# Performance work log

Measured on AMD Instinct MI355X. Metric: run time of the kernel, lower is better.

Reference implementation:

```python
import jax, jax.numpy as jnp
import numpy as np

D = 9  # nodefeat_n1 = 3 (resnet feat) + 6 (pos)


def _lstm_scan(x, Wih, Whh, bih, bhh, reverse=False):
    # x: [T, B, D] -> hidden states [T, B, D]; torch gate order i,f,g,o
    B = x.shape[1]
    def step(carry, xt):
        h, c = carry
        g = xt @ Wih.T + bih + h @ Whh.T + bhh
        i = jax.nn.sigmoid(g[:, :D])
        f = jax.nn.sigmoid(g[:, D:2*D])
        gg = jnp.tanh(g[:, 2*D:3*D])
        o = jax.nn.sigmoid(g[:, 3*D:])
        c = f * c + i * gg
        h = o * jnp.tanh(c)
        return (h, c), h
    init = (jnp.zeros((B, D), x.dtype), jnp.zeros((B, D), x.dtype))
    _, hs = jax.lax.scan(step, init, x, reverse=reverse)
    return hs


def _forward(nodes_feature, pos, attmat, msg_W, msg_b, gru_Wih, gru_Whh, gru_bih, gru_bhh,
             ro1_W, ro1_b, ro2_W, ro2_b, lf_Wih, lf_Whh, lf_bih, lf_bhh,
             lb_Wih, lb_Whh, lb_bih, lb_bhh, lr1_W, lr1_b, lr2_W, lr2_b, num_rec):
    node_feat = jnp.concatenate([nodes_feature, pos], axis=-1)  # [N,T,M,D]
    N, T, M, _ = node_feat.shape
    # valid_node_num = num_rec[b, 0] in the original code
    valid = (jnp.arange(M)[None, :] < num_rec[:, 0:1]).astype(node_feat.dtype)  # [N,M]
    att = attmat * valid[:, None, None, :]  # zero out invalid source nodes q
    src = node_feat  # message sources (h_w)
    hv = node_feat   # GRU hidden (h_v)
    hidden = node_feat
    for _ in range(2):  # iterN = 2 message-passing rounds
        msg = src @ msg_W.T + msg_b                    # [N,T,M,D] message_fc
        m = jnp.einsum('btnq,btqd->btnd', att, msg)    # attention-weighted sum over q
        # single-step GRU cell (torch gate order r,z,n)
        gx = m @ gru_Wih.T + gru_bih
        gh = hv @ gru_Whh.T + gru_bhh
        r = jax.nn.sigmoid(gx[..., :D] + gh[..., :D])
        z = jax.nn.sigmoid(gx[..., D:2*D] + gh[..., D:2*D])
        n = jnp.tanh(gx[..., 2*D:] + r * gh[..., 2*D:])
        h_new = (1.0 - z) * n + z * hv
        hidden = h_new * valid[:, None, :, None]       # invalid nodes never updated -> stay zero
        src = hidden
        hv = hidden
    vmask = valid[:, None, :, None]
    # per-frame readout (pred_label0)
    p0 = jax.nn.relu(hidden @ ro1_W.T + ro1_b) @ ro2_W.T + ro2_b
    pred_label0 = p0 * vmask
    # bidirectional LSTM over time, batched over (batch, node)
    x = hidden.transpose(1, 0, 2, 3).reshape(T, N * M, D)  # [T, N*M, D]
    hf = _lstm_scan(x, lf_Wih, lf_Whh, lf_bih, lf_bhh, reverse=False)
    hb = _lstm_scan(x, lb_Wih, lb_Whh, lb_bih, lb_bhh, reverse=True)
    out = jnp.concatenate([hf, hb], axis=-1).reshape(T, N, M, 2 * D).transpose(1, 0, 2, 3)
    p = jax.nn.relu(out @ lr1_W.T + lr1_b) @ lr2_W.T + lr2_b
    pred_label = p * vmask
    return pred_label, pred_label0


def setup_inputs() -> dict:
    key = jax.random.key(0)
    ks = jax.random.split(key, 32)
    N, T, M = 8192, 20, 6
    def u(k, shape, fan_in):
        s = 1.0 / np.sqrt(fan_in).astype(np.float32)
        return jax.random.uniform(k, shape, jnp.float32, -s, s)
    return {
        "nodes_feature": jax.random.normal(ks[0], (N, T, M, 3), jnp.float32),
        "pos": jax.random.normal(ks[1], (N, T, M, 6), jnp.float32),
        "attmat": jax.random.uniform(ks[2], (N, T, M, M), jnp.float32),
        "msg_W": u(ks[3], (D, D), D), "msg_b": u(ks[4], (D,), D),
        "gru_Wih": u(ks[5], (3 * D, D), D), "gru_Whh": u(ks[6], (3 * D, D), D),
        "gru_bih": u(ks[7], (3 * D,), D), "gru_bhh": u(ks[8], (3 * D,), D),
        "ro1_W": u(ks[9], (D, D), D), "ro1_b": u(ks[10], (D,), D),
        "ro2_W": u(ks[11], (7, D), D), "ro2_b": u(ks[12], (7,), D),
        "lf_Wih": u(ks[13], (4 * D, D), D), "lf_Whh": u(ks[14], (4 * D, D), D),
        "lf_bih": u(ks[15], (4 * D,), D), "lf_bhh": u(ks[16], (4 * D,), D),
        "lb_Wih": u(ks[17], (4 * D, D), D), "lb_Whh": u(ks[18], (4 * D, D), D),
        "lb_bih": u(ks[19], (4 * D,), D), "lb_bhh": u(ks[20], (4 * D,), D),
        "lr1_W": u(ks[21], (D, 2 * D), 2 * D), "lr1_b": u(ks[22], (D,), 2 * D),
        "lr2_W": u(ks[23], (7, D), D), "lr2_b": u(ks[24], (7,), D),
        "num_rec": jax.random.randint(ks[25], (N, T), 1, M + 1),
    }


def reference(nodes_feature, pos, attmat, msg_W, msg_b, gru_Wih, gru_Whh, gru_bih, gru_bhh,
              ro1_W, ro1_b, ro2_W, ro2_b, lf_Wih, lf_Whh, lf_bih, lf_bhh,
              lb_Wih, lb_Whh, lb_bih, lb_bhh, lr1_W, lr1_b, lr2_W, lr2_b, num_rec):
    return _forward(nodes_feature, pos, attmat, msg_W, msg_b, gru_Wih, gru_Whh, gru_bih, gru_bhh,
                    ro1_W, ro1_b, ro2_W, ro2_b, lf_Wih, lf_Whh, lf_bih, lf_bhh,
                    lb_Wih, lb_Whh, lb_bih, lb_bhh, lr1_W, lr1_b, lr2_W, lr2_b, num_rec)
```

## Files before the change

### kernel.cpp

```cpp
#include <hip/hip_runtime.h>

#define N_    8192
#define T_    20
#define M_    6
#define D_    9
#define NM_   (N_*M_)
#define NT_   (N_*T_)
#define NTM7_ (N_*T_*M_*7)

#define LOG2E 1.44269504088896f

typedef __attribute__((ext_vector_type(2))) float v2f;

__device__ __forceinline__ float sigm(float x){
    return __builtin_amdgcn_rcpf(1.f + __builtin_amdgcn_exp2f(-LOG2E * x));
}
__device__ __forceinline__ float tanh_(float x){
    return fmaf(2.f, __builtin_amdgcn_rcpf(1.f + __builtin_amdgcn_exp2f(-2.f*LOG2E * x)), -1.f);
}
__device__ __forceinline__ v2f splat(float s){ return (v2f){s, s}; }
__device__ __forceinline__ v2f sigm2(v2f x){ v2f r; r.x = sigm(x.x); r.y = sigm(x.y); return r; }
__device__ __forceinline__ v2f tanh2(v2f x){ v2f r; r.x = tanh_(x.x); r.y = tanh_(x.y); return r; }
__device__ __forceinline__ v2f relu2(v2f x){ v2f r; r.x = fmaxf(x.x,0.f); r.y = fmaxf(x.y,0.f); return r; }

__global__ __launch_bounds__(64) void k_gnn(
    const float* __restrict__ nf,
    const float* __restrict__ pos,
    const float* __restrict__ am,
    const float* __restrict__ msgW, const float* __restrict__ msgb,
    const float* __restrict__ gWih, const float* __restrict__ gWhh,
    const float* __restrict__ gbih, const float* __restrict__ gbhh,
    const float* __restrict__ ro1W, const float* __restrict__ ro1b,
    const float* __restrict__ ro2W, const float* __restrict__ ro2b,
    const int*   __restrict__ numrec,
    float* __restrict__ hid,
    float* __restrict__ out0)
{
    __shared__ v2f mbuf[11 * 58];

    const int lane = threadIdx.x & 63;
    const int g    = lane / 6;
    const int i    = lane - g * 6;
    const int gB   = g * 58;
    const bool lactive = (lane < 60);

    const int wbase = blockIdx.x * 20;
    const int ntA = lactive ? (wbase + g)      : 0;
    const int ntB = lactive ? (wbase + 10 + g) : 0;
    const int nA = ntA / T_, tA = ntA - nA * T_;
    const int nB = ntB / T_, tB = ntB - nB * T_;

    v2f s[D_];
    {
        const float* pA = nf + (size_t)ntA * 18 + i * 3;
        const float* pB = nf + (size_t)ntB * 18 + i * 3;
        #pragma unroll
        for (int k = 0; k < 3; ++k) { s[k].x = pA[k]; s[k].y = pB[k]; }
    }
    {
        const float2* pA = (const float2*)(pos + (size_t)ntA * 36 + i * 6);
        const float2* pB = (const float2*)(pos + (size_t)ntB * 36 + i * 6);
        #pragma unroll
        for (int k = 0; k < 3; ++k) {
            float2 a = pA[k], b = pB[k];
            s[3 + 2*k]     = (v2f){a.x, b.x};
            s[3 + 2*k + 1] = (v2f){a.y, b.y};
        }
    }
    v2f attr[M_];
    {
        const float2* pA = (const float2*)(am + (size_t)ntA * 36 + i * 6);
        const float2* pB = (const float2*)(am + (size_t)ntB * 36 + i * 6);
        #pragma unroll
        for (int k = 0; k < 3; ++k) {
            float2 a = pA[k], b = pB[k];
            attr[2*k]     = (v2f){a.x, b.x};
            attr[2*k + 1] = (v2f){a.y, b.y};
        }
    }
    const int nrA = numrec[nA * T_];
    const int nrB = numrec[nB * T_];
    #pragma unroll
    for (int q = 0; q < M_; ++q) {
        attr[q].x *= (q < nrA) ? 1.f : 0.f;
        attr[q].y *= (q < nrB) ? 1.f : 0.f;
    }
    v2f vmi; vmi.x = (i < nrA) ? 1.f : 0.f; vmi.y = (i < nrB) ? 1.f : 0.f;

    #pragma unroll
    for (int it = 0; it < 2; ++it) {
        #pragma unroll
        for (int d = 0; d < D_; ++d) {
            v2f a = splat(msgb[d]);
            #pragma unroll
            for (int k = 0; k < D_; ++k) a += s[k] * msgW[d*9 + k];
            mbuf[gB + d*6 + i] = a;
        }
        v2f mm[D_];
        #pragma unroll
        for (int d = 0; d < D_; ++d) {
            const float4* rp = (const float4*)&mbuf[gB + d*6];
            float4 p0 = rp[0], p1 = rp[1], p2 = rp[2];
            v2f a = attr[0] * (v2f){p0.x, p0.y};
            a += attr[1] * (v2f){p0.z, p0.w};
            a += attr[2] * (v2f){p1.x, p1.y};
            a += attr[3] * (v2f){p1.z, p1.w};
            a += attr[4] * (v2f){p2.x, p2.y};
            a += attr[5] * (v2f){p2.z, p2.w};
            mm[d] = a;
        }
        v2f grz[18], gxn[9], ghn[9];
        #pragma unroll
        for (int j = 0; j < 18; ++j) {
            v2f a = splat(gbih[j] + gbhh[j]);
            #pragma unroll
            for (int k = 0; k < D_; ++k) {
                a += mm[k] * gWih[j*9 + k];
                a += s[k]  * gWhh[j*9 + k];
            }
            grz[j] = a;
        }
        #pragma unroll
        for (int j = 0; j < 9; ++j) {
            v2f ax = splat(gbih[18 + j]), ah = splat(gbhh[18 + j]);
            #pragma unroll
            for (int k = 0; k < D_; ++k) {
                ax += mm[k] * gWih[(18 + j)*9 + k];
                ah += s[k]  * gWhh[(18 + j)*9 + k];
            }
            gxn[j] = ax; ghn[j] = ah;
        }
        #pragma unroll
        for (int d = 0; d < D_; ++d) {
            v2f r  = sigm2(grz[d]);
            v2f z  = sigm2(grz[9 + d]);
            v2f nn = tanh2(gxn[d] + r * ghn[d]);
            s[d] = vmi * ((splat(1.f) - z) * nn + z * s[d]);
        }
    }

    if (lactive) {
        float* hpA = hid + (size_t)(nA * M_ + i) * (T_ * D_) + tA * D_;
        float* hpB = hid + (size_t)(nB * M_ + i) * (T_ * D_) + tB * D_;
        #pragma unroll
        for (int d = 0; d < D_; ++d) { hpA[d] = s[d].x; hpB[d] = s[d].y; }
    }

    v2f q9[D_];
    #pragma unroll
    for (int d = 0; d < D_; ++d) {
        v2f a = splat(ro1b[d]);
        #pragma unroll
        for (int k = 0; k < D_; ++k) a += s[k] * ro1W[d*9 + k];
        q9[d] = relu2(a);
    }
    if (lactive) {
        float* opA = out0 + (size_t)ntA * 42 + i * 7;
        float* opB = out0 + (size_t)ntB * 42 + i * 7;
        #pragma unroll
        for (int j = 0; j < 7; ++j) {
            v2f a = splat(ro2b[j]);
            #pragma unroll
            for (int k = 0; k < D_; ++k) a += q9[k] * ro2W[j*9 + k];
            a *= vmi;
            opA[j] = a.x; opB[j] = a.y;
        }
    }
}

#define CPB 14

__global__ __launch_bounds__(128) void k_lstm(
    const float* __restrict__ hid,
    const float* __restrict__ fWih, const float* __restrict__ fWhh,
    const float* __restrict__ fbih, const float* __restrict__ fbhh,
    const float* __restrict__ bWih, const float* __restrict__ bWhh,
    const float* __restrict__ bbih, const float* __restrict__ bbhh,
    const float* __restrict__ lr1W, const float* __restrict__ lr1b,
    const float* __restrict__ lr2W, const float* __restrict__ lr2b,
    const int*   __restrict__ numrec,
    float* __restrict__ out)
{
    __shared__ float hst[16 * 404];
    __shared__ float hxs[16 * 20];

    const int lane = threadIdx.x & 63;
    const int wib  = threadIdx.x >> 6;
    const int grp0 = lane / 9;
    const int d    = lane - grp0 * 9;
    const int row  = wib * 8 + grp0;
    const int grp  = (grp0 < 7) ? grp0 : 6;

    bool active = (lane < 63);
    int ci = blockIdx.x * CPB + wib * 7 + grp;
    active = active && (ci < NM_);
    const int nm = active ? ci : 0;

    const float* xb = hid + (size_t)nm * (T_ * D_);
    const int crow = row * 20;
    const int hrow = row * 404;

    {
        float wxi[9], wxf[9], wxg[9], wxo[9], whi[9], whf[9], whg[9], who[9];
        #pragma unroll
        for (int k = 0; k < 9; ++k) {
            wxi[k] = fWih[(d     )*9 + k];  whi[k] = fWhh[(d     )*9 + k];
            wxf[k] = fWih[(9  + d)*9 + k];  whf[k] = fWhh[(9  + d)*9 + k];
            wxg[k] = fWih[(18 + d)*9 + k];  whg[k] = fWhh[(18 + d)*9 + k];
            wxo[k] = fWih[(27 + d)*9 + k];  who[k] = fWhh[(27 + d)*9 + k];
        }
        const float bi = fbih[d]      + fbhh[d];
        const float bf = fbih[9 + d]  + fbhh[9 + d];
        const float bg = fbih[18 + d] + fbhh[18 + d];
        const float bo = fbih[27 + d] + fbhh[27 + d];

        hxs[crow + 2*d] = 0.f;
        float h = 0.f, c = 0.f;
        for (int t = 0; t < T_; ++t) {
            hxs[crow + 2*d + 1] = xb[t*9 + d];
            float gi = bi, gf = bf, gg = bg, go = bo;
            #pragma unroll
            for (int j = 0; j < 8; j += 2) {
                float4 v = *(const float4*)&hxs[crow + 2*j];
                gi = fmaf(v.x, whi[j], fmaf(v.y, wxi[j], gi));
                gf = fmaf(v.x, whf[j], fmaf(v.y, wxf[j], gf));
                gg = fmaf(v.x, whg[j], fmaf(v.y, wxg[j], gg));
                go = fmaf(v.x, who[j], fmaf(v.y, wxo[j], go));
                gi = fmaf(v.z, whi[j+1], fmaf(v.w, wxi[j+1], gi));
                gf = fmaf(v.z, whf[j+1], fmaf(v.w, wxf[j+1], gf));
                gg = fmaf(v.z, whg[j+1], fmaf(v.w, wxg[j+1], gg));
                go = fmaf(v.z, who[j+1], fmaf(v.w, wxo[j+1], go));
            }
            {
                float2 v = *(const float2*)&hxs[crow + 16];
                gi = fmaf(v.x, whi[8], fmaf(v.y, wxi[8], gi));
                gf = fmaf(v.x, whf[8], fmaf(v.y, wxf[8], gf));
                gg = fmaf(v.x, whg[8], fmaf(v.y, wxg[8], gg));
                go = fmaf(v.x, who[8], fmaf(v.y, wxo[8], go));
            }
            c = sigm(gf) * c + sigm(gi) * tanh_(gg);
            h = sigm(go) * tanh_(c);
            hst[hrow + t*20 + d] = h;
            hxs[crow + 2*d] = h;
        }
    }

    {
        float wxi[9], wxf[9], wxg[9], wxo[9], whi[9], whf[9], whg[9], who[9];
        #pragma unroll
        for (int k = 0; k < 9; ++k) {
            wxi[k] = bWih[(d     )*9 + k];  whi[k] = bWhh[(d     )*9 + k];
            wxf[k] = bWih[(9  + d)*9 + k];  whf[k] = bWhh[(9  + d)*9 + k];
            wxg[k] = bWih[(18 + d)*9 + k];  whg[k] = bWhh[(18 + d)*9 + k];
            wxo[k] = bWih[(27 + d)*9 + k];  who[k] = bWhh[(27 + d)*9 + k];
        }
        const float bi = bbih[d]      + bbhh[d];
        const float bf = bbih[9 + d]  + bbhh[9 + d];
        const float bg = bbih[18 + d] + bbhh[18 + d];
        const float bo = bbih[27 + d] + bbhh[27 + d];

        hxs[crow + 2*d] = 0.f;
        float h = 0.f, c = 0.f;
        for (int tt = T_ - 1; tt >= 0; --tt) {
            hxs[crow + 2*d + 1] = xb[tt*9 + d];
            float gi = bi, gf = bf, gg = bg, go = bo;
            #pragma unroll
            for (int j = 0; j < 8; j += 2) {
                float4 v = *(const float4*)&hxs[crow + 2*j];
                gi = fmaf(v.x, whi[j], fmaf(v.y, wxi[j], gi));
                gf = fmaf(v.x, whf[j], fmaf(v.y, wxf[j], gf));
                gg = fmaf(v.x, whg[j], fmaf(v.y, wxg[j], gg));
                go = fmaf(v.x, who[j], fmaf(v.y, wxo[j], go));
                gi = fmaf(v.z, whi[j+1], fmaf(v.w, wxi[j+1], gi));
                gf = fmaf(v.z, whf[j+1], fmaf(v.w, wxf[j+1], gf));
                gg = fmaf(v.z, whg[j+1], fmaf(v.w, wxg[j+1], gg));
                go = fmaf(v.z, who[j+1], fmaf(v.w, wxo[j+1], go));
            }
            {
                float2 v = *(const float2*)&hxs[crow + 16];
                gi = fmaf(v.x, whi[8], fmaf(v.y, wxi[8], gi));
                gf = fmaf(v.x, whf[8], fmaf(v.y, wxf[8], gf));
                gg = fmaf(v.x, whg[8], fmaf(v.y, wxg[8], gg));
                go = fmaf(v.x, who[8], fmaf(v.y, wxo[8], go));
            }
            c = sigm(gf) * c + sigm(gi) * tanh_(gg);
            h = sigm(go) * tanh_(c);
            hst[hrow + tt*20 + 10 + d] = h;
            hxs[crow + 2*d] = h;
        }
    }

    #pragma unroll 1
    for (int rr = 0; rr < 3; ++rr) {
        const int item = rr * 64 + lane;
        if (item >= 140) break;
        const int ch = item / 20;
        const int t  = item - ch * 20;
        const int ci2 = blockIdx.x * CPB + wib * 7 + ch;
        if (ci2 >= NM_) continue;
        const int base = (wib * 8 + ch) * 404 + t * 20;

        float hf[9], hb[9];
        #pragma unroll
        for (int j = 0; j < 4; ++j) {
            float2 a = *(const float2*)&hst[base + 2*j];
            hf[2*j] = a.x; hf[2*j+1] = a.y;
            float2 b = *(const float2*)&hst[base + 10 + 2*j];
            hb[2*j] = b.x; hb[2*j+1] = b.y;
        }
        hf[8] = hst[base + 8];
        hb[8] = hst[base + 18];

        const int n2 = ci2 / M_;
        const int m2 = ci2 - n2 * M_;
        const float vi = (m2 < numrec[n2 * T_]) ? 1.f : 0.f;

        float q[9];
        #pragma unroll
        for (int dd = 0; dd < 9; ++dd) {
            float a = lr1b[dd];
            #pragma unroll
            for (int k = 0; k < 9; ++k) a = fmaf(hf[k], lr1W[dd*18 + k], a);
            #pragma unroll
            for (int k = 0; k < 9; ++k) a = fmaf(hb[k], lr1W[dd*18 + 9 + k], a);
            q[dd] = fmaxf(a, 0.f);
        }
        float* op = out + (size_t)((n2 * T_ + t) * M_ + m2) * 7;
        #pragma unroll
        for (int j = 0; j < 7; ++j) {
            float a = lr2b[j];
            #pragma unroll
            for (int k = 0; k < 9; ++k) a = fmaf(q[k], lr2W[j*9 + k], a);
            op[j] = a * vi;
        }
    }
}

extern "C" void kernel_launch(void* const* d_in, const int* in_sizes, int n_in,
                              void* d_out, int out_size, void* d_ws, size_t ws_size,
                              hipStream_t stream) {
    const float* nf    = (const float*)d_in[0];
    const float* pos   = (const float*)d_in[1];
    const float* am    = (const float*)d_in[2];
    const float* msgW  = (const float*)d_in[3];
    const float* msgb  = (const float*)d_in[4];
    const float* gWih  = (const float*)d_in[5];
    const float* gWhh  = (const float*)d_in[6];
    const float* gbih  = (const float*)d_in[7];
    const float* gbhh  = (const float*)d_in[8];
    const float* ro1W  = (const float*)d_in[9];
    const float* ro1b  = (const float*)d_in[10];
    const float* ro2W  = (const float*)d_in[11];
    const float* ro2b  = (const float*)d_in[12];
    const float* lfWih = (const float*)d_in[13];
    const float* lfWhh = (const float*)d_in[14];
    const float* lfbih = (const float*)d_in[15];
    const float* lfbhh = (const float*)d_in[16];
    const float* lbWih = (const float*)d_in[17];
    const float* lbWhh = (const float*)d_in[18];
    const float* lbbih = (const float*)d_in[19];
    const float* lbbhh = (const float*)d_in[20];
    const float* lr1W  = (const float*)d_in[21];
    const float* lr1b  = (const float*)d_in[22];
    const float* lr2W  = (const float*)d_in[23];
    const float* lr2b  = (const float*)d_in[24];
    const int* numrec  = (const int*)d_in[25];

    float* hid = (float*)d_ws;

    float* outp = (float*)d_out;
    float* out0 = (float*)d_out + NTM7_;

    k_gnn <<<NT_ / 20, 64, 0, stream>>>(nf, pos, am, msgW, msgb, gWih, gWhh,
                                        gbih, gbhh, ro1W, ro1b, ro2W, ro2b,
                                        numrec, hid, out0);
    const int lgrid = (NM_ + CPB - 1) / CPB;
    k_lstm<<<lgrid, 128, 0, stream>>>(hid, lfWih, lfWhh, lfbih, lfbhh,
                                      lbWih, lbWhh, lbbih, lbbhh,
                                      lr1W, lr1b, lr2W, lr2b, numrec, outp);
}
```

Before: 291.5 us.

## Process two LSTM chains per lane with packed float2 math and prefetched inputs

The LSTM kernel now gives each lane a pair of (batch,node) chains and runs the gate math as two-wide vectors (v2f), so each weight register feeds two sequences and packed FMA can be used. The next timestep's input is loaded from global memory before the current step's math, taking that load off the serial recurrence. Blocks shrink to one 64-thread wave handling 7 pairs, with the shared-memory layout changed to float4/v2f rows. This halves the number of lanes and waves, which may hurt latency hiding, and raises register use per lane.

```diff
diff --git a/kernel.cpp b/kernel.cpp
--- a/kernel.cpp
+++ b/kernel.cpp
@@ -5,6 +5,7 @@
 #define M_    6
 #define D_    9
 #define NM_   (N_*M_)
+#define NMP_  (NM_/2)
 #define NT_   (N_*T_)
 #define NTM7_ (N_*T_*M_*7)
 
@@ -168,9 +169,7 @@
     }
 }
 
-#define CPB 14
-
-__global__ __launch_bounds__(128) void k_lstm(
+__global__ __launch_bounds__(64) void k_lstm(
     const float* __restrict__ hid,
     const float* __restrict__ fWih, const float* __restrict__ fWhh,
     const float* __restrict__ fbih, const float* __restrict__ fbhh,
@@ -181,24 +180,24 @@
     const int*   __restrict__ numrec,
     float* __restrict__ out)
 {
-    __shared__ float hst[16 * 404];
-    __shared__ float hxs[16 * 20];
+    __shared__ float4 hxs4[8 * 11];
+    __shared__ v2f    hstv[8 * 381];
 
     const int lane = threadIdx.x & 63;
-    const int wib  = threadIdx.x >> 6;
     const int grp0 = lane / 9;
     const int d    = lane - grp0 * 9;
-    const int row  = wib * 8 + grp0;
-    const int grp  = (grp0 < 7) ? grp0 : 6;
-
-    bool active = (lane < 63);
-    int ci = blockIdx.x * CPB + wib * 7 + grp;
-    active = active && (ci < NM_);
-    const int nm = active ? ci : 0;
-
-    const float* xb = hid + (size_t)nm * (T_ * D_);
-    const int crow = row * 20;
-    const int hrow = row * 404;
+    const int row  = grp0;
+
+    bool active = (grp0 < 7);
+    int pi = blockIdx.x * 7 + (active ? grp0 : 0);
+    active = active && (pi < NMP_);
+    const int pair = active ? pi : 0;
+    const int cA = pair * 2, cB = cA + 1;
+
+    const float* xbA = hid + (size_t)cA * (T_ * D_);
+    const float* xbB = hid + (size_t)cB * (T_ * D_);
+    const int xrow = row * 11;
+    const int hrow = row * 381;
 
     {
         float wxi[9], wxf[9], wxg[9], wxo[9], whi[9], whf[9], whg[9], who[9];
@@ -214,34 +213,25 @@
         const float bg = fbih[18 + d] + fbhh[18 + d];
         const float bo = fbih[27 + d] + fbhh[27 + d];
 
-        hxs[crow + 2*d] = 0.f;
-        float h = 0.f, c = 0.f;
+        hxs4[xrow + d] = make_float4(0.f, 0.f, xbA[d], xbB[d]);
+        v2f h = splat(0.f), c = splat(0.f);
         for (int t = 0; t < T_; ++t) {
-            hxs[crow + 2*d + 1] = xb[t*9 + d];
-            float gi = bi, gf = bf, gg = bg, go = bo;
-            #pragma unroll
-            for (int j = 0; j < 8; j += 2) {
-                float4 v = *(const float4*)&hxs[crow + 2*j];
-                gi = fmaf(v.x, whi[j], fmaf(v.y, wxi[j], gi));
-                gf = fmaf(v.x, whf[j], fmaf(v.y, wxf[j], gf));
-                gg = fmaf(v.x, whg[j], fmaf(v.y, wxg[j], gg));
-                go = fmaf(v.x, who[j], fmaf(v.y, wxo[j], go));
-                gi = fmaf(v.z, whi[j+1], fmaf(v.w, wxi[j+1], gi));
-                gf = fmaf(v.z, whf[j+1], fmaf(v.w, wxf[j+1], gf));
-                gg = fmaf(v.z, whg[j+1], fmaf(v.w, wxg[j+1], gg));
-                go = fmaf(v.z, who[j+1], fmaf(v.w, wxo[j+1], go));
+            const float xnA = (t < T_-1) ? xbA[(t+1)*9 + d] : 0.f;
+            const float xnB = (t < T_-1) ? xbB[(t+1)*9 + d] : 0.f;
+            v2f gi = splat(bi), gf = splat(bf), gg = splat(bg), go = splat(bo);
+            #pragma unroll
+            for (int j = 0; j < 9; ++j) {
+                float4 v = hxs4[xrow + j];
+                v2f hj = (v2f){v.x, v.y}, xj = (v2f){v.z, v.w};
+                gi += hj * whi[j]; gi += xj * wxi[j];
+                gf += hj * whf[j]; gf += xj * wxf[j];
+                gg += hj * whg[j]; gg += xj * wxg[j];
+                go += hj * who[j]; go += xj * wxo[j];
             }
-            {
-                float2 v = *(const float2*)&hxs[crow + 16];
-                gi = fmaf(v.x, whi[8], fmaf(v.y, wxi[8], gi));
-                gf = fmaf(v.x, whf[8], fmaf(v.y, wxf[8], gf));
-                gg = fmaf(v.x, whg[8], fmaf(v.y, wxg[8], gg));
-                go = fmaf(v.x, who[8], fmaf(v.y, wxo[8], go));
-            }
-            c = sigm(gf) * c + sigm(gi) * tanh_(gg);
-            h = sigm(go) * tanh_(c);
-            hst[hrow + t*20 + d] = h;
-            hxs[crow + 2*d] = h;
+            c = sigm2(gf) * c + sigm2(gi) * tanh2(gg);
+            h = sigm2(go) * tanh2(c);
+            hstv[hrow + t*19 + d] = h;
+            hxs4[xrow + d] = make_float4(h.x, h.y, xnA, xnB);
         }
     }
 
@@ -259,34 +249,25 @@
         const float bg = bbih[18 + d] + bbhh[18 + d];
         const float bo = bbih[27 + d] + bbhh[27 + d];
 
-        hxs[crow + 2*d] = 0.f;
-        float h = 0.f, c = 0.f;
+        hxs4[xrow + d] = make_float4(0.f, 0.f, xbA[19*9 + d], xbB[19*9 + d]);
+        v2f h = splat(0.f), c = splat(0.f);
         for (int tt = T_ - 1; tt >= 0; --tt) {
-            hxs[crow + 2*d + 1] = xb[tt*9 + d];
-            float gi = bi, gf = bf, gg = bg, go = bo;
-            #pragma unroll
-            for (int j = 0; j < 8; j += 2) {
-                float4 v = *(const float4*)&hxs[crow + 2*j];
-                gi = fmaf(v.x, whi[j], fmaf(v.y, wxi[j], gi));
-                gf = fmaf(v.x, whf[j], fmaf(v.y, wxf[j], gf));
-                gg = fmaf(v.x, whg[j], fmaf(v.y, wxg[j], gg));
-                go = fmaf(v.x, who[j], fmaf(v.y, wxo[j], go));
-                gi = fmaf(v.z, whi[j+1], fmaf(v.w, wxi[j+1], gi));
-                gf = fmaf(v.z, whf[j+1], fmaf(v.w, wxf[j+1], gf));
-                gg = fmaf(v.z, whg[j+1], fmaf(v.w, wxg[j+1], gg));
-                go = fmaf(v.z, who[j+1], fmaf(v.w, wxo[j+1], go));
+            const float xnA = (tt > 0) ? xbA[(tt-1)*9 + d] : 0.f;
+            const float xnB = (tt > 0) ? xbB[(tt-1)*9 + d] : 0.f;
+            v2f gi = splat(bi), gf = splat(bf), gg = splat(bg), go = splat(bo);
+            #pragma unroll
+            for (int j = 0; j < 9; ++j) {
+                float4 v = hxs4[xrow + j];
+                v2f hj = (v2f){v.x, v.y}, xj = (v2f){v.z, v.w};
+                gi += hj * whi[j]; gi += xj * wxi[j];
+                gf += hj * whf[j]; gf += xj * wxf[j];
+                gg += hj * whg[j]; gg += xj * wxg[j];
+                go += hj * who[j]; go += xj * wxo[j];
             }
-            {
-                float2 v = *(const float2*)&hxs[crow + 16];
-                gi = fmaf(v.x, whi[8], fmaf(v.y, wxi[8], gi));
-                gf = fmaf(v.x, whf[8], fmaf(v.y, wxf[8], gf));
-                gg = fmaf(v.x, whg[8], fmaf(v.y, wxg[8], gg));
-                go = fmaf(v.x, who[8], fmaf(v.y, wxo[8], go));
-            }
-            c = sigm(gf) * c + sigm(gi) * tanh_(gg);
-            h = sigm(go) * tanh_(c);
-            hst[hrow + tt*20 + 10 + d] = h;
-            hxs[crow + 2*d] = h;
+            c = sigm2(gf) * c + sigm2(gi) * tanh2(gg);
+            h = sigm2(go) * tanh2(c);
+            hstv[hrow + tt*19 + 9 + d] = h;
+            hxs4[xrow + d] = make_float4(h.x, h.y, xnA, xnB);
         }
     }
 
@@ -296,42 +277,40 @@
         if (item >= 140) break;
         const int ch = item / 20;
         const int t  = item - ch * 20;
-        const int ci2 = blockIdx.x * CPB + wib * 7 + ch;
-        if (ci2 >= NM_) continue;
-        const int base = (wib * 8 + ch) * 404 + t * 20;
-
-        float hf[9], hb[9];
-        #pragma unroll
-        for (int j = 0; j < 4; ++j) {
-            float2 a = *(const float2*)&hst[base + 2*j];
-            hf[2*j] = a.x; hf[2*j+1] = a.y;
-            float2 b = *(const float2*)&hst[base + 10 + 2*j];
-            hb[2*j] = b.x; hb[2*j+1] = b.y;
-        }
-        hf[8] = hst[base + 8];
-        hb[8] = hst[base + 18];
-
-        const int n2 = ci2 / M_;
-        const int m2 = ci2 - n2 * M_;
-        const float vi = (m2 < numrec[n2 * T_]) ? 1.f : 0.f;
-
-        float q[9];
+        const int pi2 = blockIdx.x * 7 + ch;
+        if (pi2 >= NMP_) continue;
+        const int base = ch * 381 + t * 19;
+
+        v2f hf[9], hb[9];
+        #pragma unroll
+        for (int k = 0; k < 9; ++k) { hf[k] = hstv[base + k]; hb[k] = hstv[base + 9 + k]; }
+
+        const int cA2 = pi2 * 2, cB2 = cA2 + 1;
+        const int nA2 = cA2 / M_, mA2 = cA2 - nA2 * M_;
+        const int nB2 = cB2 / M_, mB2 = cB2 - nB2 * M_;
+        v2f vi;
+        vi.x = (mA2 < numrec[nA2 * T_]) ? 1.f : 0.f;
+        vi.y = (mB2 < numrec[nB2 * T_]) ? 1.f : 0.f;
+
+        v2f q[9];
         #pragma unroll
         for (int dd = 0; dd < 9; ++dd) {
-            float a = lr1b[dd];
-            #pragma unroll
-            for (int k = 0; k < 9; ++k) a = fmaf(hf[k], lr1W[dd*18 + k], a);
-            #pragma unroll
-            for (int k = 0; k < 9; ++k) a = fmaf(hb[k], lr1W[dd*18 + 9 + k], a);
-            q[dd] = fmaxf(a, 0.f);
-        }
-        float* op = out + (size_t)((n2 * T_ + t) * M_ + m2) * 7;
+            v2f a = splat(lr1b[dd]);
+            #pragma unroll
+            for (int k = 0; k < 9; ++k) a += hf[k] * lr1W[dd*18 + k];
+            #pragma unroll
+            for (int k = 0; k < 9; ++k) a += hb[k] * lr1W[dd*18 + 9 + k];
+            q[dd] = relu2(a);
+        }
+        float* opA = out + (size_t)((nA2 * T_ + t) * M_ + mA2) * 7;
+        float* opB = out + (size_t)((nB2 * T_ + t) * M_ + mB2) * 7;
         #pragma unroll
         for (int j = 0; j < 7; ++j) {
-            float a = lr2b[j];
-            #pragma unroll
-            for (int k = 0; k < 9; ++k) a = fmaf(q[k], lr2W[j*9 + k], a);
-            op[j] = a * vi;
+            v2f a = splat(lr2b[j]);
+            #pragma unroll
+            for (int k = 0; k < 9; ++k) a += q[k] * lr2W[j*9 + k];
+            a *= vi;
+            opA[j] = a.x; opB[j] = a.y;
         }
     }
 }
@@ -374,8 +353,8 @@
     k_gnn <<<NT_ / 20, 64, 0, stream>>>(nf, pos, am, msgW, msgb, gWih, gWhh,
                                         gbih, gbhh, ro1W, ro1b, ro2W, ro2b,
                                         numrec, hid, out0);
-    const int lgrid = (NM_ + CPB - 1) / CPB;
-    k_lstm<<<lgrid, 128, 0, stream>>>(hid, lfWih, lfWhh, lfbih, lfbhh,
-                                      lbWih, lbWhh, lbbih, lbbhh,
-                                      lr1W, lr1b, lr2W, lr2b, numrec, outp);
-}
+    const int lgrid = (NMP_ + 6) / 7;
+    k_lstm<<<lgrid, 64, 0, stream>>>(hid, lfWih, lfWhh, lfbih, lfbhh,
+                                     lbWih, lbWhh, lbbih, lbbhh,
+                                     lr1W, lr1b, lr2W, lr2b, numrec, outp);
+}
```

After: 287.9 us. Within noise of the previous version (-1.2%).
